# Optimization experiments

Hardware: AMD Instinct MI355X
Metric: run time of the kernel (lower is better)

## Reference

```python
import jax, jax.numpy as jnp
import numpy as np
from jax import lax

SMOOTH = 1e-06
THRESH_WIDTH = 10


def _max_pool3(x):
    # 3x3 max pool, stride 1, padding 1 (torch pads with -inf for max pool)
    return lax.reduce_window(x, -jnp.inf, lax.max,
                             (1, 1, 3, 3), (1, 1, 1, 1),
                             [(0, 0), (0, 0), (1, 1), (1, 1)])


def soft_skeletonize(x):
    def body(x, _):
        min_pool = -_max_pool3(-x)
        contour = jax.nn.relu(_max_pool3(min_pool) - min_pool)
        return jax.nn.relu(x - contour), None
    x, _ = lax.scan(body, x, None, length=THRESH_WIDTH)
    return x


def norm_intersection(center_line, vessel):
    smooth = 1.0
    b, c = center_line.shape[:2]
    clf = center_line.reshape(b, c, -1)
    vf = vessel.reshape(b, c, -1)
    intersection = (clf * vf).sum(-1)
    return (intersection + smooth) / (clf.sum(-1) + smooth)


def dice_loss(pred, target):
    intersection = (pred * target).sum()
    denominator = pred.sum() + target.sum()
    dice_score = (2.0 * intersection + SMOOTH) / (denominator + SMOOTH)
    return 1.0 - dice_score


def soft_cldice_loss(pred, target):
    cl_pred = soft_skeletonize(pred)
    target_skeleton = soft_skeletonize(target)
    iflat = norm_intersection(cl_pred, target)
    tflat = norm_intersection(target_skeleton, pred)
    intersection = (iflat * tflat).sum()
    return 1.0 - 2.0 * intersection / (iflat + tflat).sum()


def setup_inputs() -> dict:
    key = jax.random.key(0)
    k1, k2 = jax.random.split(key)
    shape = (64, 1, 512, 512)
    pred = jax.random.uniform(k1, shape, dtype=jnp.float32)
    target = jax.random.uniform(k2, shape, dtype=jnp.float32)
    return {"pred": pred, "target": target}


def reference(pred, target):
    return 0.8 * dice_loss(pred, target) + 0.2 * soft_cldice_loss(pred, target)
```

## Files before the change

### kernel.cpp

```cpp
#include <hip/hip_runtime.h>


#define H 512
#define W 512
#define NIMG 64
#define TOT 128
#define IMG_ELEMS (H * W)
#define RSTRIPS 32
#define SROWS (H / RSTRIPS)
#define NDICE_SLOTS 64

__device__ float g_A[(size_t)TOT * IMG_ELEMS];
__device__ float g_B[(size_t)TOT * IMG_ELEMS];
__device__ float g_acc[NIMG * 4];
__device__ float g_dice[NDICE_SLOTS * 16];

#define SEL_A 2
#define SEL_B 3

struct F8 { float4 a, b; };

__device__ __forceinline__ F8 f8fill(float v) {
  F8 r; r.a = make_float4(v, v, v, v); r.b = r.a; return r;
}
__device__ __forceinline__ F8 f8min(const F8& x, const F8& y) {
  F8 r;
  r.a.x = fminf(x.a.x, y.a.x); r.a.y = fminf(x.a.y, y.a.y);
  r.a.z = fminf(x.a.z, y.a.z); r.a.w = fminf(x.a.w, y.a.w);
  r.b.x = fminf(x.b.x, y.b.x); r.b.y = fminf(x.b.y, y.b.y);
  r.b.z = fminf(x.b.z, y.b.z); r.b.w = fminf(x.b.w, y.b.w);
  return r;
}
__device__ __forceinline__ F8 f8max(const F8& x, const F8& y) {
  F8 r;
  r.a.x = fmaxf(x.a.x, y.a.x); r.a.y = fmaxf(x.a.y, y.a.y);
  r.a.z = fmaxf(x.a.z, y.a.z); r.a.w = fmaxf(x.a.w, y.a.w);
  r.b.x = fmaxf(x.b.x, y.b.x); r.b.y = fmaxf(x.b.y, y.b.y);
  r.b.z = fmaxf(x.b.z, y.b.z); r.b.w = fmaxf(x.b.w, y.b.w);
  return r;
}
__device__ __forceinline__ F8 ero8(const F8& v, int lane) {
  float L = __shfl_up(v.b.w, 1, 64);
  if (lane == 0) L = __builtin_inff();
  float R = __shfl_down(v.a.x, 1, 64);
  if (lane == 63) R = __builtin_inff();
  F8 e;
  e.a.x = fminf(L,     fminf(v.a.x, v.a.y));
  e.a.y = fminf(v.a.x, fminf(v.a.y, v.a.z));
  e.a.z = fminf(v.a.y, fminf(v.a.z, v.a.w));
  e.a.w = fminf(v.a.z, fminf(v.a.w, v.b.x));
  e.b.x = fminf(v.a.w, fminf(v.b.x, v.b.y));
  e.b.y = fminf(v.b.x, fminf(v.b.y, v.b.z));
  e.b.z = fminf(v.b.y, fminf(v.b.z, v.b.w));
  e.b.w = fminf(v.b.z, fminf(v.b.w, R));
  return e;
}
__device__ __forceinline__ F8 dil8(const F8& v, int lane) {
  float L = __shfl_up(v.b.w, 1, 64);
  if (lane == 0) L = -__builtin_inff();
  float R = __shfl_down(v.a.x, 1, 64);
  if (lane == 63) R = -__builtin_inff();
  F8 d;
  d.a.x = fmaxf(L,     fmaxf(v.a.x, v.a.y));
  d.a.y = fmaxf(v.a.x, fmaxf(v.a.y, v.a.z));
  d.a.z = fmaxf(v.a.y, fmaxf(v.a.z, v.a.w));
  d.a.w = fmaxf(v.a.z, fmaxf(v.a.w, v.b.x));
  d.b.x = fmaxf(v.a.w, fmaxf(v.b.x, v.b.y));
  d.b.y = fmaxf(v.b.x, fmaxf(v.b.y, v.b.z));
  d.b.z = fmaxf(v.b.y, fmaxf(v.b.z, v.b.w));
  d.b.w = fmaxf(v.b.z, fmaxf(v.b.w, R));
  return d;
}
__device__ __forceinline__ F8 f8relu_sub(const F8& x, const F8& y) {
  F8 r;
  r.a.x = fmaxf(x.a.x - y.a.x, 0.f); r.a.y = fmaxf(x.a.y - y.a.y, 0.f);
  r.a.z = fmaxf(x.a.z - y.a.z, 0.f); r.a.w = fmaxf(x.a.w - y.a.w, 0.f);
  r.b.x = fmaxf(x.b.x - y.b.x, 0.f); r.b.y = fmaxf(x.b.y - y.b.y, 0.f);
  r.b.z = fmaxf(x.b.z - y.b.z, 0.f); r.b.w = fmaxf(x.b.w - y.b.w, 0.f);
  return r;
}
__device__ __forceinline__ float f8dot(const F8& x, const float4& oa,
                                       const float4& ob) {
  return x.a.x * oa.x + x.a.y * oa.y + x.a.z * oa.z + x.a.w * oa.w
       + x.b.x * ob.x + x.b.y * ob.y + x.b.z * ob.z + x.b.w * ob.w;
}
__device__ __forceinline__ float f8sum(const F8& x) {
  return x.a.x + x.a.y + x.a.z + x.a.w + x.b.x + x.b.y + x.b.z + x.b.w;
}

template <int MODE>
__device__ __forceinline__ void skel2_core(
    const float* __restrict__ simg, float* __restrict__ dimg,
    const float* __restrict__ oimg, bool isPred, int r0, int lane,
    float out3[3]) {
  const float PINF = __builtin_inff();
  float a0 = 0.f, a1 = 0.f, a2 = 0.f;

  auto loadrow = [&](int r) -> F8 {
    F8 v;
    if (r >= 0 && r < H) {
      const float4* rp = (const float4*)(simg + (size_t)r * W);
      v.a = rp[lane * 2];
      v.b = rp[lane * 2 + 1];
      if (MODE == 1 && r >= r0 && r < r0 + SROWS) {
        if (isPred) {
          const float4* tp = (const float4*)(oimg + (size_t)r * W);
          float4 ta = tp[lane * 2], tb = tp[lane * 2 + 1];
          a0 += f8dot(v, ta, tb);
          a1 += f8sum(v);
        } else {
          a2 += f8sum(v);
        }
      }
    } else {
      v = f8fill(PINF);
    }
    return v;
  };

  int s = r0 - 2;
  F8 xa = loadrow(s - 2);
  F8 xb = loadrow(s - 1);
  F8 xc = loadrow(s);
  F8 xp = loadrow(s + 1);
  F8 xn = loadrow(s + 2);
  F8 em = ero8(f8min(xa, f8min(xb, xc)), lane);
  if (s - 1 < 0) em = f8fill(-PINF);
  F8 ec = ero8(f8min(xb, f8min(xc, xp)), lane);
  if (s < 0) ec = f8fill(-PINF);
  F8 pmaxA = f8max(em, ec);
  F8 pminA = f8min(xc, xp);

  auto step1 = [&]() -> F8 {
    F8 ep = ero8(f8min(pminA, xn), lane);
    if (s + 1 < 0 || s + 1 >= H) ep = f8fill(-PINF);
    F8 dil = dil8(f8max(pmaxA, ep), lane);
    F8 y = f8relu_sub(xc, f8relu_sub(dil, ec));
    if (s < 0 || s >= H) y = f8fill(PINF);
    pminA = f8min(xp, xn);
    pmaxA = f8max(ec, ep);
    xc = xp; xp = xn; xn = loadrow(s + 3);
    ec = ep;
    ++s;
    return y;
  };

  F8 ya = step1();
  F8 yb = step1();
  F8 yc = step1();
  F8 yp = step1();
  F8 yn = step1();
  F8 e2m = ero8(f8min(ya, f8min(yb, yc)), lane);
  if (r0 - 1 < 0) e2m = f8fill(-PINF);
  F8 e2c = ero8(f8min(yb, f8min(yc, yp)), lane);
  F8 pmax2 = f8max(e2m, e2c);
  F8 pmin2 = f8min(yc, yp);

  #pragma unroll 2
  for (int t = r0; t < r0 + SROWS; ++t) {
    F8 ynew = step1();
    F8 e2p = ero8(f8min(pmin2, yn), lane);
    if (t + 1 >= H) e2p = f8fill(-PINF);
    F8 d2 = dil8(f8max(pmax2, e2p), lane);
    F8 z = f8relu_sub(yc, f8relu_sub(d2, e2c));

    if (MODE == 2) {
      const float4* orp = (const float4*)(oimg + (size_t)t * W);
      float4 oa = orp[lane * 2];
      float4 ob = orp[lane * 2 + 1];
      a0 += f8dot(z, oa, ob);
      a1 += f8sum(z);
    } else {
      float4* op = (float4*)(dimg + (size_t)t * W);
      op[lane * 2]     = z.a;
      op[lane * 2 + 1] = z.b;
    }
    pmin2 = f8min(yp, yn);
    pmax2 = f8max(e2c, e2p);
    yc = yp; yp = yn; yn = ynew; e2c = e2p;
  }

  if (MODE != 0) {
    #pragma unroll
    for (int o = 32; o; o >>= 1) {
      a0 += __shfl_down(a0, o, 64);
      a1 += __shfl_down(a1, o, 64);
      if (MODE == 1) a2 += __shfl_down(a2, o, 64);
    }
    out3[0] = a0; out3[1] = a1; out3[2] = a2;
  }
}

__global__ __launch_bounds__(256) void pass_start(
    const float* __restrict__ pred, const float* __restrict__ target) {
  const int wid  = blockIdx.x * 4 + (threadIdx.x >> 6);
  const int lane = threadIdx.x & 63;
  const int u    = wid / RSTRIPS;
  const int r0   = (wid % RSTRIPS) * SROWS;
  const bool isPred = (u < NIMG);
  const float* src = isPred ? pred + (size_t)u * IMG_ELEMS
                            : target + (size_t)(u - NIMG) * IMG_ELEMS;
  const float* o = isPred ? target + (size_t)u * IMG_ELEMS : nullptr;
  float* dst = (float*)g_A + (size_t)u * IMG_ELEMS;

  float out3[3] = {0.f, 0.f, 0.f};
  skel2_core<1>(src, dst, o, isPred, r0, lane, out3);

  __shared__ float red[4][3];
  const int wave = threadIdx.x >> 6;
  if (lane == 0) {
    red[wave][0] = out3[0]; red[wave][1] = out3[1]; red[wave][2] = out3[2];
  }
  __syncthreads();
  if (threadIdx.x < 3) {
    float sv = red[0][threadIdx.x] + red[1][threadIdx.x] +
               red[2][threadIdx.x] + red[3][threadIdx.x];
    atomicAdd(&g_dice[(blockIdx.x & (NDICE_SLOTS - 1)) * 16 + threadIdx.x], sv);
  }
}

__global__ __launch_bounds__(256) void pass_plain(int srcSel) {
  const float* src = (srcSel == SEL_A) ? (const float*)g_A : (const float*)g_B;
  float* dst = (srcSel == SEL_A) ? g_B : g_A;
  const int wid  = blockIdx.x * 4 + (threadIdx.x >> 6);
  const int lane = threadIdx.x & 63;
  const int u    = wid / RSTRIPS;
  const int r0   = (wid % RSTRIPS) * SROWS;
  skel2_core<0>(src + (size_t)u * IMG_ELEMS, dst + (size_t)u * IMG_ELEMS,
                nullptr, false, r0, lane, nullptr);
}

__global__ __launch_bounds__(256) void pass_reduce(
    const float* __restrict__ pred, const float* __restrict__ target) {
  const int wid  = blockIdx.x * 4 + (threadIdx.x >> 6);
  const int lane = threadIdx.x & 63;
  const int u    = wid / RSTRIPS;
  const int r0   = (wid % RSTRIPS) * SROWS;
  const bool isPred = (u < NIMG);
  const int img = isPred ? u : u - NIMG;
  const int accBase = isPred ? 0 : 2;
  const float* src = (const float*)g_B + (size_t)u * IMG_ELEMS;
  const float* o = isPred ? target + (size_t)img * IMG_ELEMS
                          : pred + (size_t)img * IMG_ELEMS;

  float out3[3] = {0.f, 0.f, 0.f};
  skel2_core<2>(src, nullptr, o, isPred, r0, lane, out3);

  __shared__ float red[4][2];
  const int wave = threadIdx.x >> 6;
  if (lane == 0) { red[wave][0] = out3[0]; red[wave][1] = out3[1]; }
  __syncthreads();
  if (threadIdx.x < 2) {
    float sv = red[0][threadIdx.x] + red[1][threadIdx.x] +
               red[2][threadIdx.x] + red[3][threadIdx.x];
    atomicAdd(&g_acc[img * 4 + accBase + threadIdx.x], sv);
  }
}

__global__ void zero_acc() {
  for (int i = threadIdx.x; i < NIMG * 4; i += 256) g_acc[i] = 0.0f;
  for (int i = threadIdx.x; i < NDICE_SLOTS * 16; i += 256) g_dice[i] = 0.0f;
}

__global__ void final_kernel(float* __restrict__ out) {
  const int lane = threadIdx.x;
  float s1 = g_acc[lane * 4 + 0], s2 = g_acc[lane * 4 + 1];
  float s3 = g_acc[lane * 4 + 2], s4 = g_acc[lane * 4 + 3];
  float iflat = (s1 + 1.0f) / (s2 + 1.0f);
  float tflat = (s3 + 1.0f) / (s4 + 1.0f);
  float prod = iflat * tflat;
  float ssum = iflat + tflat;
  float d0 = g_dice[lane * 16 + 0];
  float d1 = g_dice[lane * 16 + 1];
  float d2 = g_dice[lane * 16 + 2];
  #pragma unroll
  for (int o = 32; o; o >>= 1) {
    prod += __shfl_down(prod, o, 64);
    ssum += __shfl_down(ssum, o, 64);
    d0   += __shfl_down(d0, o, 64);
    d1   += __shfl_down(d1, o, 64);
    d2   += __shfl_down(d2, o, 64);
  }
  if (lane == 0) {
    float cldice = 1.0f - 2.0f * prod / ssum;
    float dice = 1.0f - (2.0f * d0 + 1e-6f) / (d1 + d2 + 1e-6f);
    out[0] = 0.8f * dice + 0.2f * cldice;
  }
}

extern "C" void kernel_launch(void* const* d_in, const int* in_sizes, int n_in,
                              void* d_out, int out_size, void* d_ws, size_t ws_size,
                              hipStream_t stream) {
  const float* pred   = (const float*)d_in[0];
  const float* target = (const float*)d_in[1];
  float* out = (float*)d_out;
  (void)d_ws; (void)ws_size;

  const int nblocks = TOT * RSTRIPS / 4;

  zero_acc<<<1, 256, 0, stream>>>();
  pass_start<<<nblocks, 256, 0, stream>>>(pred, target);
  pass_plain<<<nblocks, 256, 0, stream>>>(SEL_A);
  pass_plain<<<nblocks, 256, 0, stream>>>(SEL_B);
  pass_plain<<<nblocks, 256, 0, stream>>>(SEL_A);
  pass_reduce<<<nblocks, 256, 0, stream>>>(pred, target);
  final_kernel<<<1, 64, 0, stream>>>(out);
}
```

Before: 433.0 us.

## Fuse all skeletonize iterations into one LDS-resident tiled kernel with halo recompute

Replaces the five global-memory passes (start, three plain, reduce) with one kernel. Each 1024-thread block loads an 80-row strip plus halo of one image into shared memory, runs all ten erode/dilate iterations in place, and computes the dice and clDice partial sums from that tile. This removes the repeated full-image reads and writes of the intermediate buffers and the extra kernel launches. In exchange the halo rows are computed twice, each block occupies most of a CU's LDS so occupancy is low, and every iteration adds block-wide barriers. A 64-row tile variant is used if the larger shared-memory request is refused.

```diff
diff --git a/kernel.cpp b/kernel.cpp
--- a/kernel.cpp
+++ b/kernel.cpp
@@ -3,20 +3,14 @@
 
 #define H 512
 #define W 512
+#define W4 (W / 4)
 #define NIMG 64
-#define TOT 128
 #define IMG_ELEMS (H * W)
-#define RSTRIPS 32
-#define SROWS (H / RSTRIPS)
 #define NDICE_SLOTS 64
-
-__device__ float g_A[(size_t)TOT * IMG_ELEMS];
-__device__ float g_B[(size_t)TOT * IMG_ELEMS];
+#define ITERS 10
+
 __device__ float g_acc[NIMG * 4];
 __device__ float g_dice[NDICE_SLOTS * 16];
-
-#define SEL_A 2
-#define SEL_B 3
 
 struct F8 { float4 a, b; };
 
@@ -71,6 +65,14 @@
   d.b.w = fmaxf(v.b.z, fmaxf(v.b.w, R));
   return d;
 }
+__device__ __forceinline__ F8 f8sub(const F8& x, const F8& y) {
+  F8 r;
+  r.a.x = x.a.x - y.a.x; r.a.y = x.a.y - y.a.y;
+  r.a.z = x.a.z - y.a.z; r.a.w = x.a.w - y.a.w;
+  r.b.x = x.b.x - y.b.x; r.b.y = x.b.y - y.b.y;
+  r.b.z = x.b.z - y.b.z; r.b.w = x.b.w - y.b.w;
+  return r;
+}
 __device__ __forceinline__ F8 f8relu_sub(const F8& x, const F8& y) {
   F8 r;
   r.a.x = fmaxf(x.a.x - y.a.x, 0.f); r.a.y = fmaxf(x.a.y - y.a.y, 0.f);
@@ -79,181 +81,133 @@
   r.b.z = fmaxf(x.b.z - y.b.z, 0.f); r.b.w = fmaxf(x.b.w - y.b.w, 0.f);
   return r;
 }
-__device__ __forceinline__ float f8dot(const F8& x, const float4& oa,
-                                       const float4& ob) {
-  return x.a.x * oa.x + x.a.y * oa.y + x.a.z * oa.z + x.a.w * oa.w
-       + x.b.x * ob.x + x.b.y * ob.y + x.b.z * ob.z + x.b.w * ob.w;
-}
-__device__ __forceinline__ float f8sum(const F8& x) {
-  return x.a.x + x.a.y + x.a.z + x.a.w + x.b.x + x.b.y + x.b.z + x.b.w;
-}
-
-template <int MODE>
-__device__ __forceinline__ void skel2_core(
-    const float* __restrict__ simg, float* __restrict__ dimg,
-    const float* __restrict__ oimg, bool isPred, int r0, int lane,
-    float out3[3]) {
+
+template <int TROWS, int RR>
+__global__ __launch_bounds__(1024) void mega(
+    const float* __restrict__ pred, const float* __restrict__ target) {
+  extern __shared__ float tile[];
+  constexpr int NSTRIP = (H + RR - 1) / RR;
+  constexpr int HALO = (TROWS - RR) / 2;
+  constexpr int CH = TROWS / 16;
   const float PINF = __builtin_inff();
-  float a0 = 0.f, a1 = 0.f, a2 = 0.f;
-
-  auto loadrow = [&](int r) -> F8 {
-    F8 v;
-    if (r >= 0 && r < H) {
-      const float4* rp = (const float4*)(simg + (size_t)r * W);
-      v.a = rp[lane * 2];
-      v.b = rp[lane * 2 + 1];
-      if (MODE == 1 && r >= r0 && r < r0 + SROWS) {
-        if (isPred) {
-          const float4* tp = (const float4*)(oimg + (size_t)r * W);
-          float4 ta = tp[lane * 2], tb = tp[lane * 2 + 1];
-          a0 += f8dot(v, ta, tb);
-          a1 += f8sum(v);
-        } else {
-          a2 += f8sum(v);
-        }
+
+  const int u     = blockIdx.x / NSTRIP;
+  const int strip = blockIdx.x % NSTRIP;
+  const int g0    = strip * RR;
+  const int nown  = min(H - g0, RR);
+  const bool isPred = (u < NIMG);
+  const int img  = isPred ? u : u - NIMG;
+  const float* src   = (isPred ? pred : target) + (size_t)img * IMG_ELEMS;
+  const float* other = (isPred ? target : pred) + (size_t)img * IMG_ELEMS;
+
+  const int tid  = threadIdx.x;
+  const int lane = tid & 63;
+  const int wave = tid >> 6;
+  const int gbase = g0 - HALO;
+
+  {
+    const float4* s4 = (const float4*)src;
+    float4* t4 = (float4*)tile;
+    for (int i = tid; i < TROWS * W4; i += 1024) {
+      int gr = gbase + (i >> 7);
+      if (gr >= 0 && gr < H) t4[i] = s4[(size_t)gr * W4 + (i & 127)];
+    }
+  }
+  __syncthreads();
+
+  {
+    float a0 = 0.f, a1 = 0.f;
+    const float4* o4 = (const float4*)(other + (size_t)g0 * W);
+    const float4* x4 = (const float4*)(tile + (size_t)HALO * W);
+    for (int i = tid; i < nown * W4; i += 1024) {
+      float4 x = x4[i];
+      if (isPred) {
+        float4 t = o4[i];
+        a0 += x.x * t.x + x.y * t.y + x.z * t.z + x.w * t.w;
+        a1 += x.x + x.y + x.z + x.w;
+      } else {
+        a0 += x.x + x.y + x.z + x.w;
       }
-    } else {
-      v = f8fill(PINF);
-    }
-    return v;
-  };
-
-  int s = r0 - 2;
-  F8 xa = loadrow(s - 2);
-  F8 xb = loadrow(s - 1);
-  F8 xc = loadrow(s);
-  F8 xp = loadrow(s + 1);
-  F8 xn = loadrow(s + 2);
-  F8 em = ero8(f8min(xa, f8min(xb, xc)), lane);
-  if (s - 1 < 0) em = f8fill(-PINF);
-  F8 ec = ero8(f8min(xb, f8min(xc, xp)), lane);
-  if (s < 0) ec = f8fill(-PINF);
-  F8 pmaxA = f8max(em, ec);
-  F8 pminA = f8min(xc, xp);
-
-  auto step1 = [&]() -> F8 {
-    F8 ep = ero8(f8min(pminA, xn), lane);
-    if (s + 1 < 0 || s + 1 >= H) ep = f8fill(-PINF);
-    F8 dil = dil8(f8max(pmaxA, ep), lane);
-    F8 y = f8relu_sub(xc, f8relu_sub(dil, ec));
-    if (s < 0 || s >= H) y = f8fill(PINF);
-    pminA = f8min(xp, xn);
-    pmaxA = f8max(ec, ep);
-    xc = xp; xp = xn; xn = loadrow(s + 3);
-    ec = ep;
-    ++s;
-    return y;
-  };
-
-  F8 ya = step1();
-  F8 yb = step1();
-  F8 yc = step1();
-  F8 yp = step1();
-  F8 yn = step1();
-  F8 e2m = ero8(f8min(ya, f8min(yb, yc)), lane);
-  if (r0 - 1 < 0) e2m = f8fill(-PINF);
-  F8 e2c = ero8(f8min(yb, f8min(yc, yp)), lane);
-  F8 pmax2 = f8max(e2m, e2c);
-  F8 pmin2 = f8min(yc, yp);
-
-  #pragma unroll 2
-  for (int t = r0; t < r0 + SROWS; ++t) {
-    F8 ynew = step1();
-    F8 e2p = ero8(f8min(pmin2, yn), lane);
-    if (t + 1 >= H) e2p = f8fill(-PINF);
-    F8 d2 = dil8(f8max(pmax2, e2p), lane);
-    F8 z = f8relu_sub(yc, f8relu_sub(d2, e2c));
-
-    if (MODE == 2) {
-      const float4* orp = (const float4*)(oimg + (size_t)t * W);
-      float4 oa = orp[lane * 2];
-      float4 ob = orp[lane * 2 + 1];
-      a0 += f8dot(z, oa, ob);
-      a1 += f8sum(z);
-    } else {
-      float4* op = (float4*)(dimg + (size_t)t * W);
-      op[lane * 2]     = z.a;
-      op[lane * 2 + 1] = z.b;
-    }
-    pmin2 = f8min(yp, yn);
-    pmax2 = f8max(e2c, e2p);
-    yc = yp; yp = yn; yn = ynew; e2c = e2p;
-  }
-
-  if (MODE != 0) {
+    }
     #pragma unroll
     for (int o = 32; o; o >>= 1) {
       a0 += __shfl_down(a0, o, 64);
       a1 += __shfl_down(a1, o, 64);
-      if (MODE == 1) a2 += __shfl_down(a2, o, 64);
-    }
-    out3[0] = a0; out3[1] = a1; out3[2] = a2;
-  }
-}
-
-__global__ __launch_bounds__(256) void pass_start(
-    const float* __restrict__ pred, const float* __restrict__ target) {
-  const int wid  = blockIdx.x * 4 + (threadIdx.x >> 6);
-  const int lane = threadIdx.x & 63;
-  const int u    = wid / RSTRIPS;
-  const int r0   = (wid % RSTRIPS) * SROWS;
-  const bool isPred = (u < NIMG);
-  const float* src = isPred ? pred + (size_t)u * IMG_ELEMS
-                            : target + (size_t)(u - NIMG) * IMG_ELEMS;
-  const float* o = isPred ? target + (size_t)u * IMG_ELEMS : nullptr;
-  float* dst = (float*)g_A + (size_t)u * IMG_ELEMS;
-
-  float out3[3] = {0.f, 0.f, 0.f};
-  skel2_core<1>(src, dst, o, isPred, r0, lane, out3);
-
-  __shared__ float red[4][3];
-  const int wave = threadIdx.x >> 6;
-  if (lane == 0) {
-    red[wave][0] = out3[0]; red[wave][1] = out3[1]; red[wave][2] = out3[2];
+    }
+    if (lane == 0) {
+      float* slot = &g_dice[(blockIdx.x & (NDICE_SLOTS - 1)) * 16];
+      if (isPred) { atomicAdd(slot + 0, a0); atomicAdd(slot + 1, a1); }
+      else        { atomicAdd(slot + 2, a0); }
+    }
+  }
+
+  const int tb = wave * CH;
+  auto ldrow = [&](int tr) -> F8 {
+    int gr = gbase + tr;
+    F8 v;
+    if (gr >= 0 && gr < H) {
+      int trc = tr < 0 ? 0 : (tr >= TROWS ? TROWS - 1 : tr);
+      const float4* p = (const float4*)(tile + (size_t)trc * W);
+      v.a = p[lane * 2]; v.b = p[lane * 2 + 1];
+    } else {
+      v = f8fill(PINF);
+    }
+    return v;
+  };
+  auto erow = [&](const F8& x0, const F8& x1, const F8& x2, int tr) -> F8 {
+    F8 e = ero8(f8min(f8min(x0, x1), x2), lane);
+    int gr = gbase + tr;
+    if (gr < 0 || gr >= H) e = f8fill(-PINF);
+    return e;
+  };
+
+  for (int k = 0; k < ITERS; ++k) {
+    __syncthreads();
+    F8 xm = ldrow(tb - 2);
+    F8 xc = ldrow(tb - 1);
+    F8 xp = ldrow(tb);
+    F8 eM = erow(xm, xc, xp, tb - 1);
+    F8 xq = ldrow(tb + 1);
+    F8 eC = erow(xc, xp, xq, tb);
+    F8 y[CH];
+    #pragma unroll
+    for (int i = 0; i < CH; ++i) {
+      F8 xn = ldrow(tb + 2 + i);
+      F8 eP = erow(xp, xq, xn, tb + 1 + i);
+      F8 d  = dil8(f8max(f8max(eM, eC), eP), lane);
+      y[i]  = f8relu_sub(xp, f8sub(d, eC));
+      xp = xq; xq = xn; eM = eC; eC = eP;
+    }
+    __syncthreads();
+    #pragma unroll
+    for (int i = 0; i < CH; ++i) {
+      float4* p = (float4*)(tile + (size_t)(tb + i) * W);
+      p[lane * 2]     = y[i].a;
+      p[lane * 2 + 1] = y[i].b;
+    }
   }
   __syncthreads();
-  if (threadIdx.x < 3) {
-    float sv = red[0][threadIdx.x] + red[1][threadIdx.x] +
-               red[2][threadIdx.x] + red[3][threadIdx.x];
-    atomicAdd(&g_dice[(blockIdx.x & (NDICE_SLOTS - 1)) * 16 + threadIdx.x], sv);
-  }
-}
-
-__global__ __launch_bounds__(256) void pass_plain(int srcSel) {
-  const float* src = (srcSel == SEL_A) ? (const float*)g_A : (const float*)g_B;
-  float* dst = (srcSel == SEL_A) ? g_B : g_A;
-  const int wid  = blockIdx.x * 4 + (threadIdx.x >> 6);
-  const int lane = threadIdx.x & 63;
-  const int u    = wid / RSTRIPS;
-  const int r0   = (wid % RSTRIPS) * SROWS;
-  skel2_core<0>(src + (size_t)u * IMG_ELEMS, dst + (size_t)u * IMG_ELEMS,
-                nullptr, false, r0, lane, nullptr);
-}
-
-__global__ __launch_bounds__(256) void pass_reduce(
-    const float* __restrict__ pred, const float* __restrict__ target) {
-  const int wid  = blockIdx.x * 4 + (threadIdx.x >> 6);
-  const int lane = threadIdx.x & 63;
-  const int u    = wid / RSTRIPS;
-  const int r0   = (wid % RSTRIPS) * SROWS;
-  const bool isPred = (u < NIMG);
-  const int img = isPred ? u : u - NIMG;
-  const int accBase = isPred ? 0 : 2;
-  const float* src = (const float*)g_B + (size_t)u * IMG_ELEMS;
-  const float* o = isPred ? target + (size_t)img * IMG_ELEMS
-                          : pred + (size_t)img * IMG_ELEMS;
-
-  float out3[3] = {0.f, 0.f, 0.f};
-  skel2_core<2>(src, nullptr, o, isPred, r0, lane, out3);
-
-  __shared__ float red[4][2];
-  const int wave = threadIdx.x >> 6;
-  if (lane == 0) { red[wave][0] = out3[0]; red[wave][1] = out3[1]; }
-  __syncthreads();
-  if (threadIdx.x < 2) {
-    float sv = red[0][threadIdx.x] + red[1][threadIdx.x] +
-               red[2][threadIdx.x] + red[3][threadIdx.x];
-    atomicAdd(&g_acc[img * 4 + accBase + threadIdx.x], sv);
+
+  {
+    float b0 = 0.f, b1 = 0.f;
+    const float4* o4 = (const float4*)(other + (size_t)g0 * W);
+    const float4* x4 = (const float4*)(tile + (size_t)HALO * W);
+    for (int i = tid; i < nown * W4; i += 1024) {
+      float4 x = x4[i];
+      float4 t = o4[i];
+      b0 += x.x * t.x + x.y * t.y + x.z * t.z + x.w * t.w;
+      b1 += x.x + x.y + x.z + x.w;
+    }
+    #pragma unroll
+    for (int o = 32; o; o >>= 1) {
+      b0 += __shfl_down(b0, o, 64);
+      b1 += __shfl_down(b1, o, 64);
+    }
+    if (lane == 0) {
+      const int base = img * 4 + (isPred ? 0 : 2);
+      atomicAdd(&g_acc[base + 0], b0);
+      atomicAdd(&g_acc[base + 1], b1);
+    }
   }
 }
 
@@ -296,13 +250,26 @@
   float* out = (float*)d_out;
   (void)d_ws; (void)ws_size;
 
-  const int nblocks = TOT * RSTRIPS / 4;
+  static int use80 = -1;
+  if (use80 < 0) {
+    hipError_t e = hipFuncSetAttribute(
+        reinterpret_cast<const void*>(mega<80, 40>),
+        hipFuncAttributeMaxDynamicSharedMemorySize, 80 * W * 4);
+    use80 = (e == hipSuccess) ? 1 : 0;
+    if (!use80) {
+      (void)hipFuncSetAttribute(
+          reinterpret_cast<const void*>(mega<64, 24>),
+          hipFuncAttributeMaxDynamicSharedMemorySize, 64 * W * 4);
+    }
+  }
 
   zero_acc<<<1, 256, 0, stream>>>();
-  pass_start<<<nblocks, 256, 0, stream>>>(pred, target);
-  pass_plain<<<nblocks, 256, 0, stream>>>(SEL_A);
-  pass_plain<<<nblocks, 256, 0, stream>>>(SEL_B);
-  pass_plain<<<nblocks, 256, 0, stream>>>(SEL_A);
-  pass_reduce<<<nblocks, 256, 0, stream>>>(pred, target);
+  if (use80) {
+    constexpr int NSTRIP = (H + 39) / 40;
+    mega<80, 40><<<128 * NSTRIP, 1024, 80 * W * 4, stream>>>(pred, target);
+  } else {
+    constexpr int NSTRIP = (H + 23) / 24;
+    mega<64, 24><<<128 * NSTRIP, 1024, 64 * W * 4, stream>>>(pred, target);
+  }
   final_kernel<<<1, 64, 0, stream>>>(out);
 }
```

After: 625.1 us. 44.4% more time.

## Generalize temporal skeleton fusion to K iterations per pass, cutting passes from five to three

Applied to the files above, without the earlier changes.

Replaces the fixed two-iteration streaming skeletonization core with a templated K-stage cascade that keeps per-stage row windows in registers. Passes now fuse 4, 4 and 2 iterations, so intermediate images go through global memory fewer times and fewer kernels are launched. Strips grow from 16 to 32 rows to amortize the larger halo recompute, and launch bounds request 2 blocks per CU. In exchange it raises register pressure, adds redundant halo work and gives less parallelism, since there are now half as many waves.

```diff
diff --git a/kernel.cpp b/kernel.cpp
--- a/kernel.cpp
+++ b/kernel.cpp
@@ -6,17 +6,14 @@
 #define NIMG 64
 #define TOT 128
 #define IMG_ELEMS (H * W)
-#define RSTRIPS 32
-#define SROWS (H / RSTRIPS)
+#define SROWS 32
+#define NSTRIPS (H / SROWS)
 #define NDICE_SLOTS 64
 
 __device__ float g_A[(size_t)TOT * IMG_ELEMS];
 __device__ float g_B[(size_t)TOT * IMG_ELEMS];
 __device__ float g_acc[NIMG * 4];
 __device__ float g_dice[NDICE_SLOTS * 16];
-
-#define SEL_A 2
-#define SEL_B 3
 
 struct F8 { float4 a, b; };
 
@@ -71,6 +68,14 @@
   d.b.w = fmaxf(v.b.z, fmaxf(v.b.w, R));
   return d;
 }
+__device__ __forceinline__ F8 f8sub(const F8& x, const F8& y) {
+  F8 r;
+  r.a.x = x.a.x - y.a.x; r.a.y = x.a.y - y.a.y;
+  r.a.z = x.a.z - y.a.z; r.a.w = x.a.w - y.a.w;
+  r.b.x = x.b.x - y.b.x; r.b.y = x.b.y - y.b.y;
+  r.b.z = x.b.z - y.b.z; r.b.w = x.b.w - y.b.w;
+  return r;
+}
 __device__ __forceinline__ F8 f8relu_sub(const F8& x, const F8& y) {
   F8 r;
   r.a.x = fmaxf(x.a.x - y.a.x, 0.f); r.a.y = fmaxf(x.a.y - y.a.y, 0.f);
@@ -88,18 +93,23 @@
   return x.a.x + x.a.y + x.a.z + x.a.w + x.b.x + x.b.y + x.b.z + x.b.w;
 }
 
-template <int MODE>
-__device__ __forceinline__ void skel2_core(
-    const float* __restrict__ simg, float* __restrict__ dimg,
+template <int K, int MODE>
+__device__ __forceinline__ void skelK(
+    const float* __restrict__ src, float* __restrict__ dst,
     const float* __restrict__ oimg, bool isPred, int r0, int lane,
     float out3[3]) {
   const float PINF = __builtin_inff();
   float a0 = 0.f, a1 = 0.f, a2 = 0.f;
 
+  F8 xc[K], xp[K], xn[K], eM[K], eC[K];
+  int sr[K];
+
+  int in_row = r0 - 2 * (K - 1) - 2;
+
   auto loadrow = [&](int r) -> F8 {
     F8 v;
     if (r >= 0 && r < H) {
-      const float4* rp = (const float4*)(simg + (size_t)r * W);
+      const float4* rp = (const float4*)(src + (size_t)r * W);
       v.a = rp[lane * 2];
       v.b = rp[lane * 2 + 1];
       if (MODE == 1 && r >= r0 && r < r0 + SROWS) {
@@ -118,66 +128,61 @@
     return v;
   };
 
-  int s = r0 - 2;
-  F8 xa = loadrow(s - 2);
-  F8 xb = loadrow(s - 1);
-  F8 xc = loadrow(s);
-  F8 xp = loadrow(s + 1);
-  F8 xn = loadrow(s + 2);
-  F8 em = ero8(f8min(xa, f8min(xb, xc)), lane);
-  if (s - 1 < 0) em = f8fill(-PINF);
-  F8 ec = ero8(f8min(xb, f8min(xc, xp)), lane);
-  if (s < 0) ec = f8fill(-PINF);
-  F8 pmaxA = f8max(em, ec);
-  F8 pminA = f8min(xc, xp);
-
-  auto step1 = [&]() -> F8 {
-    F8 ep = ero8(f8min(pminA, xn), lane);
-    if (s + 1 < 0 || s + 1 >= H) ep = f8fill(-PINF);
-    F8 dil = dil8(f8max(pmaxA, ep), lane);
-    F8 y = f8relu_sub(xc, f8relu_sub(dil, ec));
-    if (s < 0 || s >= H) y = f8fill(PINF);
-    pminA = f8min(xp, xn);
-    pmaxA = f8max(ec, ep);
-    xc = xp; xp = xn; xn = loadrow(s + 3);
-    ec = ep;
-    ++s;
+  auto erow = [&](const F8& x0, const F8& x1, const F8& x2, int r) -> F8 {
+    F8 e = ero8(f8min(f8min(x0, x1), x2), lane);
+    if (r < 0 || r >= H) e = f8fill(-PINF);
+    return e;
+  };
+
+  auto stepS = [&](int i, F8 in) -> F8 {
+    F8 eP = erow(xc[i], xp[i], xn[i], sr[i] + 1);
+    F8 d  = dil8(f8max(f8max(eM[i], eC[i]), eP), lane);
+    F8 y  = f8relu_sub(xc[i], f8sub(d, eC[i]));
+    if (sr[i] < 0 || sr[i] >= H) y = f8fill(PINF);
+    xc[i] = xp[i]; xp[i] = xn[i]; xn[i] = in;
+    eM[i] = eC[i]; eC[i] = eP; sr[i]++;
     return y;
   };
 
-  F8 ya = step1();
-  F8 yb = step1();
-  F8 yc = step1();
-  F8 yp = step1();
-  F8 yn = step1();
-  F8 e2m = ero8(f8min(ya, f8min(yb, yc)), lane);
-  if (r0 - 1 < 0) e2m = f8fill(-PINF);
-  F8 e2c = ero8(f8min(yb, f8min(yc, yp)), lane);
-  F8 pmax2 = f8max(e2m, e2c);
-  F8 pmin2 = f8min(yc, yp);
-
-  #pragma unroll 2
-  for (int t = r0; t < r0 + SROWS; ++t) {
-    F8 ynew = step1();
-    F8 e2p = ero8(f8min(pmin2, yn), lane);
-    if (t + 1 >= H) e2p = f8fill(-PINF);
-    F8 d2 = dil8(f8max(pmax2, e2p), lane);
-    F8 z = f8relu_sub(yc, f8relu_sub(d2, e2c));
-
+  auto cascade = [&](int m, F8 top) -> F8 {
+    F8 v = top;
+    #pragma unroll
+    for (int i = 0; i < K; ++i)
+      if (i <= m) v = stepS(i, v);
+    return v;
+  };
+
+  #pragma unroll
+  for (int j = 0; j < K; ++j) {
+    const int fj = r0 - 2 * (K - 1 - j);
+    F8 v[5];
+    #pragma unroll
+    for (int t = 0; t < 5; ++t)
+      v[t] = cascade(j - 1, loadrow(in_row++));
+    eM[j] = erow(v[0], v[1], v[2], fj - 1);
+    eC[j] = erow(v[1], v[2], v[3], fj);
+    xc[j] = v[2]; xp[j] = v[3]; xn[j] = v[4];
+    sr[j] = fj;
+  }
+
+  #pragma unroll 1
+  for (int t = 0; t < SROWS; ++t) {
+    float4 oa, ob;
     if (MODE == 2) {
-      const float4* orp = (const float4*)(oimg + (size_t)t * W);
-      float4 oa = orp[lane * 2];
-      float4 ob = orp[lane * 2 + 1];
-      a0 += f8dot(z, oa, ob);
-      a1 += f8sum(z);
+      const float4* op =
+          (const float4*)(oimg + (size_t)(r0 + t) * W);
+      oa = op[lane * 2];
+      ob = op[lane * 2 + 1];
+    }
+    F8 y = cascade(K - 1, loadrow(in_row++));
+    if (MODE == 2) {
+      a0 += f8dot(y, oa, ob);
+      a1 += f8sum(y);
     } else {
-      float4* op = (float4*)(dimg + (size_t)t * W);
-      op[lane * 2]     = z.a;
-      op[lane * 2 + 1] = z.b;
+      float4* dp = (float4*)(dst + (size_t)(r0 + t) * W);
+      dp[lane * 2]     = y.a;
+      dp[lane * 2 + 1] = y.b;
     }
-    pmin2 = f8min(yp, yn);
-    pmax2 = f8max(e2c, e2p);
-    yc = yp; yp = yn; yn = ynew; e2c = e2p;
   }
 
   if (MODE != 0) {
@@ -191,12 +196,12 @@
   }
 }
 
-__global__ __launch_bounds__(256) void pass_start(
+__global__ __launch_bounds__(256, 2) void passA(
     const float* __restrict__ pred, const float* __restrict__ target) {
   const int wid  = blockIdx.x * 4 + (threadIdx.x >> 6);
   const int lane = threadIdx.x & 63;
-  const int u    = wid / RSTRIPS;
-  const int r0   = (wid % RSTRIPS) * SROWS;
+  const int u    = wid / NSTRIPS;
+  const int r0   = (wid % NSTRIPS) * SROWS;
   const bool isPred = (u < NIMG);
   const float* src = isPred ? pred + (size_t)u * IMG_ELEMS
                             : target + (size_t)(u - NIMG) * IMG_ELEMS;
@@ -204,7 +209,7 @@
   float* dst = (float*)g_A + (size_t)u * IMG_ELEMS;
 
   float out3[3] = {0.f, 0.f, 0.f};
-  skel2_core<1>(src, dst, o, isPred, r0, lane, out3);
+  skelK<4, 1>(src, dst, o, isPred, r0, lane, out3);
 
   __shared__ float red[4][3];
   const int wave = threadIdx.x >> 6;
@@ -219,23 +224,22 @@
   }
 }
 
-__global__ __launch_bounds__(256) void pass_plain(int srcSel) {
-  const float* src = (srcSel == SEL_A) ? (const float*)g_A : (const float*)g_B;
-  float* dst = (srcSel == SEL_A) ? g_B : g_A;
+__global__ __launch_bounds__(256, 2) void passB() {
   const int wid  = blockIdx.x * 4 + (threadIdx.x >> 6);
   const int lane = threadIdx.x & 63;
-  const int u    = wid / RSTRIPS;
-  const int r0   = (wid % RSTRIPS) * SROWS;
-  skel2_core<0>(src + (size_t)u * IMG_ELEMS, dst + (size_t)u * IMG_ELEMS,
-                nullptr, false, r0, lane, nullptr);
-}
-
-__global__ __launch_bounds__(256) void pass_reduce(
+  const int u    = wid / NSTRIPS;
+  const int r0   = (wid % NSTRIPS) * SROWS;
+  skelK<4, 0>((const float*)g_A + (size_t)u * IMG_ELEMS,
+              (float*)g_B + (size_t)u * IMG_ELEMS,
+              nullptr, false, r0, lane, nullptr);
+}
+
+__global__ __launch_bounds__(256) void passC(
     const float* __restrict__ pred, const float* __restrict__ target) {
   const int wid  = blockIdx.x * 4 + (threadIdx.x >> 6);
   const int lane = threadIdx.x & 63;
-  const int u    = wid / RSTRIPS;
-  const int r0   = (wid % RSTRIPS) * SROWS;
+  const int u    = wid / NSTRIPS;
+  const int r0   = (wid % NSTRIPS) * SROWS;
   const bool isPred = (u < NIMG);
   const int img = isPred ? u : u - NIMG;
   const int accBase = isPred ? 0 : 2;
@@ -244,7 +248,7 @@
                           : pred + (size_t)img * IMG_ELEMS;
 
   float out3[3] = {0.f, 0.f, 0.f};
-  skel2_core<2>(src, nullptr, o, isPred, r0, lane, out3);
+  skelK<2, 2>(src, nullptr, o, isPred, r0, lane, out3);
 
   __shared__ float red[4][2];
   const int wave = threadIdx.x >> 6;
@@ -296,13 +300,11 @@
   float* out = (float*)d_out;
   (void)d_ws; (void)ws_size;
 
-  const int nblocks = TOT * RSTRIPS / 4;
+  const int nblocks = TOT * NSTRIPS / 4;
 
   zero_acc<<<1, 256, 0, stream>>>();
-  pass_start<<<nblocks, 256, 0, stream>>>(pred, target);
-  pass_plain<<<nblocks, 256, 0, stream>>>(SEL_A);
-  pass_plain<<<nblocks, 256, 0, stream>>>(SEL_B);
-  pass_plain<<<nblocks, 256, 0, stream>>>(SEL_A);
-  pass_reduce<<<nblocks, 256, 0, stream>>>(pred, target);
+  passA<<<nblocks, 256, 0, stream>>>(pred, target);
+  passB<<<nblocks, 256, 0, stream>>>();
+  passC<<<nblocks, 256, 0, stream>>>(pred, target);
   final_kernel<<<1, 64, 0, stream>>>(out);
 }
```

Result: faster. 391.4 us (-9.6%).
